# Optimization experiments

Hardware: AMD Instinct MI355X
Metric: run time of the kernel (lower is better)

## Reference

```python
import jax, jax.numpy as jnp
import numpy as np

N_NODES = 100000


def setup_inputs() -> dict:
    key = jax.random.key(0)
    k1, k2, k3, k4, k5 = jax.random.split(key, 5)
    feat = jax.random.normal(k1, (N_NODES, 128), dtype=jnp.float32)
    src = jax.random.randint(k2, (1600000,), 0, N_NODES, dtype=jnp.int32)
    dst = jax.random.randint(k3, (1600000,), 0, N_NODES, dtype=jnp.int32)
    # Xavier-uniform-like weight init
    limit = float(np.sqrt(6.0 / (128 + 128)))
    weight = jax.random.uniform(k4, (128, 128), minval=-limit, maxval=limit, dtype=jnp.float32)
    bias = jax.random.normal(k5, (128,), dtype=jnp.float32) * 0.0  # zeros per reset_parameters
    return {"feat": feat, "src": src, "dst": dst, "weight": weight, "bias": bias}


def reference(feat, src, dst, weight, bias):
    # copy_u/sum: gather source features along edges, scatter-add into destinations
    agg = jax.ops.segment_sum(feat[src], dst, num_segments=N_NODES)  # [N, in_feats]
    rst = agg @ weight  # [N, out_feats]
    # symmetric-ish degree normalization: in_degree^{-0.5}, clamped at 1
    deg = jax.ops.segment_sum(jnp.ones_like(dst, dtype=feat.dtype), dst, num_segments=N_NODES)
    norm = jnp.clip(deg, 1.0, None) ** -0.5  # [N]
    rst = rst * norm[:, None] + bias
    return rst
```

## Files before the change

kernel.cpp:

```cpp
#include <hip/hip_runtime.h>
#include <hip/hip_bf16.h>

#define CHUNK 1024
#define RR 64
#define DEPTH 64
#define WMAX 1600
typedef unsigned int uint;
typedef unsigned short ushort;

__global__ __launch_bounds__(256) void partition64(const int* __restrict__ src,
                                                   const int* __restrict__ dst,
                                                   int* __restrict__ gcur,
                                                   int2* __restrict__ staging,
                                                   int cap, int nE, int N) {
    __shared__ int2 bins[RR][DEPTH];
    __shared__ int cnt[RR];
    __shared__ int res[RR];
    const int t  = threadIdx.x;
    const int nb = gridDim.x;
    const int rounds = (nE + nb * 1024 - 1) / (nb * 1024);

    for (int rd = 0; rd < rounds; ++rd) {
        if (t < RR) cnt[t] = 0;
        __syncthreads();

        const int e4 = (rd * nb + blockIdx.x) * 1024 + t * 4;
        int s[4], d[4];
        int nv = 0;
        if (e4 + 3 < nE) {
            const int4 s4 = *reinterpret_cast<const int4*>(src + e4);
            const int4 d4 = *reinterpret_cast<const int4*>(dst + e4);
            s[0] = s4.x; s[1] = s4.y; s[2] = s4.z; s[3] = s4.w;
            d[0] = d4.x; d[1] = d4.y; d[2] = d4.z; d[3] = d4.w;
            nv = 4;
        } else {
            for (int e = e4; e < nE; ++e) { s[nv] = src[e]; d[nv] = dst[e]; ++nv; }
        }
#pragma unroll
        for (int i = 0; i < 4; ++i) {
            if (i < nv) {
                const int r = (int)(((long long)d[i] * RR) / N);
                const int pos = atomicAdd(&cnt[r], 1);
                if (pos < DEPTH) {
                    bins[r][pos] = make_int2(s[i], d[i]);
                } else {
                    const int gp = atomicAdd(&gcur[r], 1);
                    staging[(size_t)r * cap + gp] = make_int2(s[i], d[i]);
                }
            }
        }
        __syncthreads();
        if (t < RR) {
            int c = cnt[t];
            c = c < DEPTH ? c : DEPTH;
            cnt[t] = c;
            res[t] = (c > 0) ? atomicAdd(&gcur[t], c) : 0;
        }
        __syncthreads();
        {
            const int g = t >> 2;
            const int l = t & 3;
            const int c = cnt[g];
            const int b = res[g];
            for (int i = l; i < c; i += 4)
                staging[(size_t)g * cap + b + i] = bins[g][i];
        }
        __syncthreads();
    }
}

__global__ __launch_bounds__(1024) void range_build(const int2* __restrict__ staging,
                                                    const int* __restrict__ gcur,
                                                    int* __restrict__ deg,
                                                    int* __restrict__ off,
                                                    int* __restrict__ csr,
                                                    int cap, int N) {
    __shared__ int hist[WMAX];
    __shared__ int sbuf[1024];
    __shared__ int sbase;
    const int r = blockIdx.x;
    const int t = threadIdx.x;
    const int lo = (int)(((long long)r * N + RR - 1) / RR);
    const int hi = (int)(((long long)(r + 1) * N + RR - 1) / RR);
    const int W  = hi - lo;
    const int cnt = gcur[r];

    if (t < RR) sbuf[t] = gcur[t];
    for (int i = t; i < W; i += 1024) hist[i] = 0;
    __syncthreads();
    if (t == 0) {
        int b = 0;
        for (int i = 0; i < r; ++i) b += sbuf[i];
        sbase = b;
    }
    const int2* ep = staging + (size_t)r * cap;
    for (int i = t; i < cnt; i += 1024) {
        const int2 p = ep[i];
        atomicAdd(&hist[p.y - lo], 1);
    }
    __syncthreads();
    const int base = sbase;

    const int i0 = t * 2, i1 = t * 2 + 1;
    const int a = (i0 < W) ? hist[i0] : 0;
    const int b = (i1 < W) ? hist[i1] : 0;
    if (i0 < W) deg[lo + i0] = a;
    if (i1 < W) deg[lo + i1] = b;
    const int tsum = a + b;
    sbuf[t] = tsum;
    __syncthreads();
    for (int dd = 1; dd < 1024; dd <<= 1) {
        const int x = (t >= dd) ? sbuf[t - dd] : 0;
        __syncthreads();
        sbuf[t] += x;
        __syncthreads();
    }
    const int excl = sbuf[t] - tsum;
    if (i0 < W) { off[lo + i0] = base + excl;     hist[i0] = base + excl; }
    if (i1 < W) { off[lo + i1] = base + excl + a; hist[i1] = base + excl + a; }
    __syncthreads();

    for (int i = t; i < cnt; i += 1024) {
        const int2 p = ep[i];
        const int pos = atomicAdd(&hist[p.y - lo], 1);
        csr[pos] = p.x;
    }
}

__global__ __launch_bounds__(256) void gemm_h(const float* __restrict__ feat,
                                              const float* __restrict__ weight,
                                              ushort* __restrict__ h, int M) {
    __shared__ float As[64][68];
    __shared__ float Wc[64][128];
    const int t  = threadIdx.x;
    const int tx = t & 15;
    const int ty = t >> 4;
    const int row0 = blockIdx.x * 64;

    float acc[4][8];
#pragma unroll
    for (int i = 0; i < 4; ++i)
#pragma unroll
        for (int j = 0; j < 8; ++j) acc[i][j] = 0.0f;

    for (int c = 0; c < 2; ++c) {
        if (c) __syncthreads();
        {
            const int k4 = (t & 15) * 4;
            const int rbase = t >> 4;
#pragma unroll
            for (int p = 0; p < 4; ++p) {
                const int rr = rbase + p * 16;
                const int grow = row0 + rr;
                float4 v = make_float4(0.f, 0.f, 0.f, 0.f);
                if (grow < M)
                    v = *reinterpret_cast<const float4*>(&feat[(size_t)grow * 128 + c * 64 + k4]);
                *reinterpret_cast<float4*>(&As[rr][k4]) = v;
            }
        }
        {
#pragma unroll
            for (int p = 0; p < 8; ++p) {
                const int idx = (p * 256 + t) * 4;
                const int kk = idx >> 7;
                const int j = idx & 127;
                *reinterpret_cast<float4*>(&Wc[kk][j]) =
                    *reinterpret_cast<const float4*>(&weight[(c * 64 + kk) * 128 + j]);
            }
        }
        __syncthreads();

#pragma unroll 8
        for (int k = 0; k < 64; ++k) {
            float a[4];
#pragma unroll
            for (int i = 0; i < 4; ++i) a[i] = As[ty * 4 + i][k];
            const float4 b0 = *reinterpret_cast<const float4*>(&Wc[k][tx * 8 + 0]);
            const float4 b1 = *reinterpret_cast<const float4*>(&Wc[k][tx * 8 + 4]);
            const float b[8] = {b0.x, b0.y, b0.z, b0.w, b1.x, b1.y, b1.z, b1.w};
#pragma unroll
            for (int i = 0; i < 4; ++i)
#pragma unroll
                for (int j = 0; j < 8; ++j)
                    acc[i][j] = fmaf(a[i], b[j], acc[i][j]);
        }
    }

#pragma unroll
    for (int i = 0; i < 4; ++i) {
        const int grow = row0 + ty * 4 + i;
        if (grow < M) {
            union { ushort u16[8]; uint4 v; } pk;
#pragma unroll
            for (int j = 0; j < 8; ++j) {
                const uint u = __float_as_uint(acc[i][j]);
                pk.u16[j] = (ushort)((u + 0x7fffu + ((u >> 16) & 1u)) >> 16);
            }
            *reinterpret_cast<uint4*>(&h[(size_t)grow * 128 + tx * 8]) = pk.v;
        }
    }
}

__global__ __launch_bounds__(256) void aggregate_h(const ushort* __restrict__ h,
                                                   const int* __restrict__ csr,
                                                   const int* __restrict__ off,
                                                   const int* __restrict__ deg,
                                                   const float* __restrict__ bias,
                                                   float* __restrict__ out, int N) {
    const int node = (blockIdx.x * blockDim.x + threadIdx.x) >> 6;
    if (node >= N) return;
    const int lane = threadIdx.x & 63;
    const int q   = lane >> 4;
    const int sub = lane & 15;
    const int start = off[node];
    const int cnt   = deg[node];
    const int end   = start + cnt;

    float acc[8];
#pragma unroll
    for (int k = 0; k < 8; ++k) acc[k] = 0.0f;

#define UNPACK_ADD(rr)                                             \
    do {                                                           \
        acc[0] += __uint_as_float(((rr).x & 0xffffu) << 16);       \
        acc[1] += __uint_as_float((rr).x & 0xffff0000u);           \
        acc[2] += __uint_as_float(((rr).y & 0xffffu) << 16);       \
        acc[3] += __uint_as_float((rr).y & 0xffff0000u);           \
        acc[4] += __uint_as_float(((rr).z & 0xffffu) << 16);       \
        acc[5] += __uint_as_float((rr).z & 0xffff0000u);           \
        acc[6] += __uint_as_float(((rr).w & 0xffffu) << 16);       \
        acc[7] += __uint_as_float((rr).w & 0xffff0000u);           \
    } while (0)

    int j = start;
    for (; j + 15 < end; j += 16) {
        int s[4];
#pragma unroll
        for (int k = 0; k < 4; ++k) s[k] = csr[j + q + 4 * k];
        uint4 r[4];
#pragma unroll
        for (int k = 0; k < 4; ++k)
            r[k] = *reinterpret_cast<const uint4*>(h + (size_t)s[k] * 128 + sub * 8);
#pragma unroll
        for (int k = 0; k < 4; ++k) UNPACK_ADD(r[k]);
    }
    for (; j + 3 < end; j += 4) {
        const int s = csr[j + q];
        const uint4 rr = *reinterpret_cast<const uint4*>(h + (size_t)s * 128 + sub * 8);
        UNPACK_ADD(rr);
    }
    const int rem = end - j;
    if (q < rem) {
        const int s = csr[j + q];
        const uint4 rr = *reinterpret_cast<const uint4*>(h + (size_t)s * 128 + sub * 8);
        UNPACK_ADD(rr);
    }
#undef UNPACK_ADD

#pragma unroll
    for (int k = 0; k < 8; ++k) {
        acc[k] += __shfl_xor(acc[k], 16, 64);
        acc[k] += __shfl_xor(acc[k], 32, 64);
    }

    if (lane < 16) {
        const float nm = rsqrtf(fmaxf((float)cnt, 1.0f));
        const float4 b0 = *reinterpret_cast<const float4*>(bias + sub * 8 + 0);
        const float4 b1 = *reinterpret_cast<const float4*>(bias + sub * 8 + 4);
        float4 o0, o1;
        o0.x = fmaf(acc[0], nm, b0.x);
        o0.y = fmaf(acc[1], nm, b0.y);
        o0.z = fmaf(acc[2], nm, b0.z);
        o0.w = fmaf(acc[3], nm, b0.w);
        o1.x = fmaf(acc[4], nm, b1.x);
        o1.y = fmaf(acc[5], nm, b1.y);
        o1.z = fmaf(acc[6], nm, b1.z);
        o1.w = fmaf(acc[7], nm, b1.w);
        *reinterpret_cast<float4*>(out + (size_t)node * 128 + sub * 8 + 0) = o0;
        *reinterpret_cast<float4*>(out + (size_t)node * 128 + sub * 8 + 4) = o1;
    }
}

__global__ void hist_simple(const int* __restrict__ dst, int* __restrict__ deg, int nE) {
    int e = blockIdx.x * blockDim.x + threadIdx.x;
    if (e < nE) atomicAdd(&deg[dst[e]], 1);
}
__global__ void bucket_simple(const int* __restrict__ src, const int* __restrict__ dst,
                              int* __restrict__ cur, int* __restrict__ csr, int nE) {
    int e = blockIdx.x * blockDim.x + threadIdx.x;
    if (e < nE) {
        int pos = atomicAdd(&cur[dst[e]], 1);
        csr[pos] = src[e];
    }
}
__global__ __launch_bounds__(256) void scan_chunks(const int* __restrict__ deg,
                                                   int* __restrict__ off,
                                                   int* __restrict__ partials, int N) {
    __shared__ int sums[256];
    const int b = blockIdx.x, t = threadIdx.x;
    const int base = b * CHUNK + t * 4;
    int v[4];
#pragma unroll
    for (int i = 0; i < 4; ++i) v[i] = (base + i < N) ? deg[base + i] : 0;
    const int s = v[0] + v[1] + v[2] + v[3];
    sums[t] = s;
    __syncthreads();
    for (int d = 1; d < 256; d <<= 1) {
        int x = (t >= d) ? sums[t - d] : 0;
        __syncthreads();
        sums[t] += x;
        __syncthreads();
    }
    const int excl = sums[t] - s;
    if (t == 255) partials[b] = sums[255];
    int run = excl;
#pragma unroll
    for (int i = 0; i < 4; ++i) {
        if (base + i < N) off[base + i] = run;
        run += v[i];
    }
}
__global__ __launch_bounds__(256) void scan_partials(int* partials, int P) {
    __shared__ int buf[256];
    const int t = threadIdx.x;
    if (P <= 256) {
        const int v = (t < P) ? partials[t] : 0;
        buf[t] = v;
        __syncthreads();
        for (int d = 1; d < 256; d <<= 1) {
            int x = (t >= d) ? buf[t - d] : 0;
            __syncthreads();
            buf[t] += x;
            __syncthreads();
        }
        if (t < P) partials[t] = buf[t] - v;
    } else if (t == 0) {
        int acc = 0;
        for (int i = 0; i < P; ++i) { int v = partials[i]; partials[i] = acc; acc += v; }
    }
}
__global__ void add_base(int* __restrict__ off, int* __restrict__ cur,
                         const int* __restrict__ partials, int N) {
    int i = blockIdx.x * blockDim.x + threadIdx.x;
    if (i < N) {
        int o = off[i] + partials[i >> 10];
        off[i] = o;
        cur[i] = o;
    }
}
__global__ __launch_bounds__(256) void aggregate_f32(const float* __restrict__ feat,
                                                     const int* __restrict__ csr,
                                                     const int* __restrict__ off,
                                                     const int* __restrict__ deg,
                                                     float* __restrict__ out, int N) {
    const int node = (blockIdx.x * blockDim.x + threadIdx.x) >> 6;
    if (node >= N) return;
    const int lane = threadIdx.x & 63;
    const int start = off[node];
    const int end   = start + deg[node];
    const float2* feat2 = reinterpret_cast<const float2*>(feat);
    float ax = 0.0f, ay = 0.0f;
    for (int j = start; j < end; ++j) {
        const float2 v = feat2[(size_t)csr[j] * 64 + lane];
        ax += v.x;
        ay += v.y;
    }
    reinterpret_cast<float2*>(out)[(size_t)node * 64 + lane] = make_float2(ax, ay);
}
__global__ __launch_bounds__(256) void gemm_norm(const float* agg,
                                                 const float* __restrict__ weight,
                                                 const float* __restrict__ bias,
                                                 const int* __restrict__ deg,
                                                 float* out, int M) {
    __shared__ float As[64][68];
    __shared__ float Wc[64][128];
    const int t  = threadIdx.x;
    const int tx = t & 15;
    const int ty = t >> 4;
    const int row0 = blockIdx.x * 64;
    float acc[4][8];
#pragma unroll
    for (int i = 0; i < 4; ++i)
#pragma unroll
        for (int j = 0; j < 8; ++j) acc[i][j] = 0.0f;
    for (int c = 0; c < 2; ++c) {
        if (c) __syncthreads();
        {
            const int k4 = (t & 15) * 4;
            const int rbase = t >> 4;
#pragma unroll
            for (int p = 0; p < 4; ++p) {
                const int rr = rbase + p * 16;
                const int grow = row0 + rr;
                float4 v = make_float4(0.f, 0.f, 0.f, 0.f);
                if (grow < M)
                    v = *reinterpret_cast<const float4*>(&agg[(size_t)grow * 128 + c * 64 + k4]);
                *reinterpret_cast<float4*>(&As[rr][k4]) = v;
            }
        }
        {
#pragma unroll
            for (int p = 0; p < 8; ++p) {
                const int idx = (p * 256 + t) * 4;
                const int kk = idx >> 7;
                const int j = idx & 127;
                *reinterpret_cast<float4*>(&Wc[kk][j]) =
                    *reinterpret_cast<const float4*>(&weight[(c * 64 + kk) * 128 + j]);
            }
        }
        __syncthreads();
#pragma unroll 8
        for (int k = 0; k < 64; ++k) {
            float a[4];
#pragma unroll
            for (int i = 0; i < 4; ++i) a[i] = As[ty * 4 + i][k];
            const float4 b0 = *reinterpret_cast<const float4*>(&Wc[k][tx * 8 + 0]);
            const float4 b1 = *reinterpret_cast<const float4*>(&Wc[k][tx * 8 + 4]);
            const float b[8] = {b0.x, b0.y, b0.z, b0.w, b1.x, b1.y, b1.z, b1.w};
#pragma unroll
            for (int i = 0; i < 4; ++i)
#pragma unroll
                for (int j = 0; j < 8; ++j)
                    acc[i][j] = fmaf(a[i], b[j], acc[i][j]);
        }
    }
    float bcol[8];
#pragma unroll
    for (int j = 0; j < 8; ++j) bcol[j] = bias[tx * 8 + j];
#pragma unroll
    for (int i = 0; i < 4; ++i) {
        const int grow = row0 + ty * 4 + i;
        if (grow < M) {
            const float nm = rsqrtf(fmaxf((float)deg[grow], 1.0f));
            float4 o0, o1;
            o0.x = fmaf(acc[i][0], nm, bcol[0]);
            o0.y = fmaf(acc[i][1], nm, bcol[1]);
            o0.z = fmaf(acc[i][2], nm, bcol[2]);
            o0.w = fmaf(acc[i][3], nm, bcol[3]);
            o1.x = fmaf(acc[i][4], nm, bcol[4]);
            o1.y = fmaf(acc[i][5], nm, bcol[5]);
            o1.z = fmaf(acc[i][6], nm, bcol[6]);
            o1.w = fmaf(acc[i][7], nm, bcol[7]);
            *reinterpret_cast<float4*>(&out[(size_t)grow * 128 + tx * 8 + 0]) = o0;
            *reinterpret_cast<float4*>(&out[(size_t)grow * 128 + tx * 8 + 4]) = o1;
        }
    }
}

extern "C" void kernel_launch(void* const* d_in, const int* in_sizes, int n_in,
                              void* d_out, int out_size, void* d_ws, size_t ws_size,
                              hipStream_t stream) {
    const float* feat   = (const float*)d_in[0];
    const int*   src    = (const int*)d_in[1];
    const int*   dst    = (const int*)d_in[2];
    const float* weight = (const float*)d_in[3];
    const float* bias   = (const float*)d_in[4];
    float* out = (float*)d_out;

    const int nE = in_sizes[1];
    const int M  = in_sizes[0] / 128;
    const int P  = (M + CHUNK - 1) / CHUNK;

    int* degi     = (int*)d_ws;
    int* off      = degi + M;
    int* cur      = off + M;
    int* partials = cur + M;
    int* gcur     = partials + 256;
    int* csr      = gcur + RR;
    const size_t csr_end   = ((size_t)3 * M + 256 + RR + (size_t)nE) * sizeof(int);
    const size_t stage_off = (csr_end + 15) & ~(size_t)15;
    const int cap = (((nE + RR - 1) / RR + 8192) + 3) & ~3;
    int2* staging = (int2*)((char*)d_ws + stage_off);
    ushort* h     = (ushort*)staging;
    const size_t stage_bytes = (size_t)RR * cap * sizeof(int2);
    const size_t h_bytes     = (size_t)M * 128 * sizeof(ushort);
    const size_t need_big = stage_off + (stage_bytes > h_bytes ? stage_bytes : h_bytes);

    if (ws_size >= need_big) {
        hipMemsetAsync(gcur, 0, RR * sizeof(int), stream);
        partition64<<<1024, 256, 0, stream>>>(src, dst, gcur, staging, cap, nE, M);
        range_build<<<RR, 1024, 0, stream>>>(staging, gcur, degi, off, csr, cap, M);
        gemm_h<<<(M + 63) / 64, 256, 0, stream>>>(feat, weight, h, M);
        aggregate_h<<<(M + 3) / 4, 256, 0, stream>>>(h, csr, off, degi, bias, out, M);
    } else {
        hipMemsetAsync(degi, 0, (size_t)M * sizeof(int), stream);
        hist_simple<<<(nE + 255) / 256, 256, 0, stream>>>(dst, degi, nE);
        scan_chunks<<<P, 256, 0, stream>>>(degi, off, partials, M);
        scan_partials<<<1, 256, 0, stream>>>(partials, P);
        add_base<<<(M + 255) / 256, 256, 0, stream>>>(off, cur, partials, M);
        bucket_simple<<<(nE + 255) / 256, 256, 0, stream>>>(src, dst, cur, csr, nE);
        aggregate_f32<<<(M + 3) / 4, 256, 0, stream>>>(feat, csr, off, degi, out, M);
        gemm_norm<<<(M + 63) / 64, 256, 0, stream>>>(out, weight, bias, degi, out, M);
    }
}
```

Before: 269.1 us.

## Replace fp32 FMA GEMM with bf16 MFMA kernel and pre-transposed bf16 weights

```diff
diff --git a/kernel.cpp b/kernel.cpp
--- a/kernel.cpp
+++ b/kernel.cpp
@@ -7,6 +7,14 @@
 #define WMAX 1600
 typedef unsigned int uint;
 typedef unsigned short ushort;
+
+typedef __bf16 bf16x8 __attribute__((ext_vector_type(8)));
+typedef float  f32x4  __attribute__((ext_vector_type(4)));
+
+__device__ __forceinline__ ushort f2bf(float f) {
+    const uint u = __float_as_uint(f);
+    return (ushort)((u + 0x7fffu + ((u >> 16) & 1u)) >> 16);
+}
 
 __global__ __launch_bounds__(256) void partition64(const int* __restrict__ src,
                                                    const int* __restrict__ dst,
@@ -127,76 +135,87 @@
     }
 }
 
-__global__ __launch_bounds__(256) void gemm_h(const float* __restrict__ feat,
-                                              const float* __restrict__ weight,
-                                              ushort* __restrict__ h, int M) {
-    __shared__ float As[64][68];
-    __shared__ float Wc[64][128];
-    const int t  = threadIdx.x;
-    const int tx = t & 15;
-    const int ty = t >> 4;
+__global__ __launch_bounds__(256) void prep_w(const float* __restrict__ w,
+                                              ushort* __restrict__ wt) {
+    const int idx = blockIdx.x * 256 + threadIdx.x;
+    const int k = idx >> 7;
+    const int n = idx & 127;
+    wt[n * 128 + k] = f2bf(w[k * 128 + n]);
+}
+
+#define APITCH 136
+__global__ __launch_bounds__(256, 2) void gemm_mfma(const float* __restrict__ feat,
+                                                    const ushort* __restrict__ wt,
+                                                    ushort* __restrict__ h, int M) {
+    __shared__ ushort A_lds[64 * APITCH];
+    const int t    = threadIdx.x;
+    const int wave = t >> 6;
+    const int lane = t & 63;
+    const int quad = lane >> 4;
+    const int nn   = lane & 15;
     const int row0 = blockIdx.x * 64;
 
-    float acc[4][8];
-#pragma unroll
-    for (int i = 0; i < 4; ++i)
-#pragma unroll
-        for (int j = 0; j < 8; ++j) acc[i][j] = 0.0f;
-
-    for (int c = 0; c < 2; ++c) {
-        if (c) __syncthreads();
-        {
-            const int k4 = (t & 15) * 4;
-            const int rbase = t >> 4;
-#pragma unroll
-            for (int p = 0; p < 4; ++p) {
-                const int rr = rbase + p * 16;
-                const int grow = row0 + rr;
-                float4 v = make_float4(0.f, 0.f, 0.f, 0.f);
-                if (grow < M)
-                    v = *reinterpret_cast<const float4*>(&feat[(size_t)grow * 128 + c * 64 + k4]);
-                *reinterpret_cast<float4*>(&As[rr][k4]) = v;
-            }
-        }
-        {
-#pragma unroll
-            for (int p = 0; p < 8; ++p) {
-                const int idx = (p * 256 + t) * 4;
-                const int kk = idx >> 7;
-                const int j = idx & 127;
-                *reinterpret_cast<float4*>(&Wc[kk][j]) =
-                    *reinterpret_cast<const float4*>(&weight[(c * 64 + kk) * 128 + j]);
-            }
-        }
-        __syncthreads();
-
-#pragma unroll 8
-        for (int k = 0; k < 64; ++k) {
-            float a[4];
-#pragma unroll
-            for (int i = 0; i < 4; ++i) a[i] = As[ty * 4 + i][k];
-            const float4 b0 = *reinterpret_cast<const float4*>(&Wc[k][tx * 8 + 0]);
-            const float4 b1 = *reinterpret_cast<const float4*>(&Wc[k][tx * 8 + 4]);
-            const float b[8] = {b0.x, b0.y, b0.z, b0.w, b1.x, b1.y, b1.z, b1.w};
-#pragma unroll
-            for (int i = 0; i < 4; ++i)
-#pragma unroll
-                for (int j = 0; j < 8; ++j)
-                    acc[i][j] = fmaf(a[i], b[j], acc[i][j]);
-        }
-    }
-
-#pragma unroll
-    for (int i = 0; i < 4; ++i) {
-        const int grow = row0 + ty * 4 + i;
+    union UB { uint4 u; bf16x8 b; };
+    UB bfrag[8][4];
+#pragma unroll
+    for (int ct = 0; ct < 8; ++ct)
+#pragma unroll
+        for (int kc = 0; kc < 4; ++kc)
+            bfrag[ct][kc].u = *reinterpret_cast<const uint4*>(
+                wt + (ct * 16 + nn) * 128 + kc * 32 + quad * 8);
+
+#pragma unroll
+    for (int p = 0; p < 8; ++p) {
+        const int idx = p * 256 + t;
+        const int row = idx >> 5;
+        const int c4  = (idx & 31) * 4;
+        const int grow = row0 + row;
+        float4 v = make_float4(0.f, 0.f, 0.f, 0.f);
+        if (grow < M)
+            v = *reinterpret_cast<const float4*>(&feat[(size_t)grow * 128 + c4]);
+        const uint2 pk = make_uint2((uint)f2bf(v.x) | ((uint)f2bf(v.y) << 16),
+                                    (uint)f2bf(v.z) | ((uint)f2bf(v.w) << 16));
+        *reinterpret_cast<uint2*>(&A_lds[row * APITCH + c4]) = pk;
+    }
+    __syncthreads();
+
+    union UA { uint4 u; bf16x8 b; };
+    UA afrag[4];
+#pragma unroll
+    for (int kc = 0; kc < 4; ++kc)
+        afrag[kc].u = *reinterpret_cast<const uint4*>(
+            &A_lds[(wave * 16 + nn) * APITCH + kc * 32 + quad * 8]);
+
+    f32x4 acc[8];
+#pragma unroll
+    for (int ct = 0; ct < 8; ++ct) {
+        acc[ct] = (f32x4){0.f, 0.f, 0.f, 0.f};
+#pragma unroll
+        for (int kc = 0; kc < 4; ++kc)
+            acc[ct] = __builtin_amdgcn_mfma_f32_16x16x32_bf16(
+                afrag[kc].b, bfrag[ct][kc].b, acc[ct], 0, 0, 0);
+    }
+    __syncthreads();
+
+#pragma unroll
+    for (int ct = 0; ct < 8; ++ct) {
+#pragma unroll
+        for (int reg = 0; reg < 4; ++reg) {
+            const int rl = wave * 16 + quad * 4 + reg;
+            A_lds[rl * APITCH + ct * 16 + nn] = f2bf(acc[ct][reg]);
+        }
+    }
+    __syncthreads();
+
+#pragma unroll
+    for (int p = 0; p < 4; ++p) {
+        const int idx = p * 256 + t;
+        const int row = idx >> 4;
+        const int c16 = idx & 15;
+        const int grow = row0 + row;
         if (grow < M) {
-            union { ushort u16[8]; uint4 v; } pk;
-#pragma unroll
-            for (int j = 0; j < 8; ++j) {
-                const uint u = __float_as_uint(acc[i][j]);
-                pk.u16[j] = (ushort)((u + 0x7fffu + ((u >> 16) & 1u)) >> 16);
-            }
-            *reinterpret_cast<uint4*>(&h[(size_t)grow * 128 + tx * 8]) = pk.v;
+            const uint4 v = *reinterpret_cast<const uint4*>(&A_lds[row * APITCH + c16 * 8]);
+            *reinterpret_cast<uint4*>(&h[(size_t)grow * 128 + c16 * 8]) = v;
         }
     }
 }
@@ -467,8 +486,9 @@
     int* partials = cur + M;
     int* gcur     = partials + 256;
     int* csr      = gcur + RR;
-    const size_t csr_end   = ((size_t)3 * M + 256 + RR + (size_t)nE) * sizeof(int);
-    const size_t stage_off = (csr_end + 15) & ~(size_t)15;
+    ushort* wt    = (ushort*)(csr + nE);
+    const size_t wt_end    = ((size_t)3 * M + 256 + RR + (size_t)nE) * sizeof(int) + 32768;
+    const size_t stage_off = (wt_end + 15) & ~(size_t)15;
     const int cap = (((nE + RR - 1) / RR + 8192) + 3) & ~3;
     int2* staging = (int2*)((char*)d_ws + stage_off);
     ushort* h     = (ushort*)staging;
@@ -478,9 +498,10 @@
 
     if (ws_size >= need_big) {
         hipMemsetAsync(gcur, 0, RR * sizeof(int), stream);
+        prep_w<<<64, 256, 0, stream>>>(weight, wt);
         partition64<<<1024, 256, 0, stream>>>(src, dst, gcur, staging, cap, nE, M);
         range_build<<<RR, 1024, 0, stream>>>(staging, gcur, degi, off, csr, cap, M);
-        gemm_h<<<(M + 63) / 64, 256, 0, stream>>>(feat, weight, h, M);
+        gemm_mfma<<<(M + 63) / 64, 256, 0, stream>>>(feat, wt, h, M);
         aggregate_h<<<(M + 3) / 4, 256, 0, stream>>>(h, csr, off, degi, bias, out, M);
     } else {
         hipMemsetAsync(degi, 0, (size_t)M * sizeof(int), stream);
```

Result: faster. 248.7 us (-7.6%).
